# Kernel optimization log

Measured on AMD Instinct MI355X. Metric: run time of the kernel, lower is better.

## Reference

```python
import jax, jax.numpy as jnp
import numpy as np

GRID = (32, 32, 32)  # must match init grid_size


def setup_inputs() -> dict:
    key = jax.random.key(0)
    # Mimic the module's init: D = 0.01 everywhere + 0.1 on the 6x6 diagonal,
    # plus small uniform noise so the baseline exercises non-degenerate values.
    D = jax.random.uniform(key, (6, 6, *GRID), dtype=jnp.float32) * 0.02 + 0.01
    D = D.at[jnp.arange(6), jnp.arange(6)].add(0.1)
    return {"D": D, "sx": 1, "sy": 1, "sz": 1, "ex": 30, "ey": 30, "ez": 30,
            "max_iterations": 300}


def reference(D, sx, sy, sz, ex, ey, ez, max_iterations):
    """flash_wave (training path, inference=False): 300-step CA as one lax.scan.

    Returns the stacked history of phi (pre-update, as the torch loop appends
    phi at the top of each iteration): shape [max_iterations, 6, X, Y, Z].
    Early exit is emulated by freezing phi once the wave reaches (ex,ey,ez),
    so no per-step host sync is needed.
    """
    phi0 = jnp.zeros((6, *GRID), dtype=D.dtype).at[:, sx, sy, sz].set(1.0)
    active_D = D + 0.95  # inference=False branch

    def body(carry, _):
        phi, done = carry
        # 6x6 channel mixing per grid cell: 'oixyz,ixyz->oxyz'
        phi_out = jnp.einsum('oixyz,ixyz->oxyz', active_D, phi)
        pn = jnp.zeros_like(phi)
        pn = pn.at[0, 1:, :, :].set(phi_out[0, :-1, :, :])   # +x
        pn = pn.at[1, :-1, :, :].set(phi_out[1, 1:, :, :])   # -x
        pn = pn.at[2, :, 1:, :].set(phi_out[2, :, :-1, :])   # +y
        pn = pn.at[3, :, :-1, :].set(phi_out[3, :, 1:, :])   # -y
        pn = pn.at[4, :, :, 1:].set(phi_out[4, :, :, :-1])   # +z
        pn = pn.at[5, :, :, :-1].set(phi_out[5, :, :, 1:])   # -z
        nxt = jnp.clip(pn, 0.0, 1.0)
        nxt = jnp.where(done, phi, nxt)  # freeze after target reached
        reached = jnp.sum(nxt[:, ex, ey, ez]) > 0.01
        return (nxt, jnp.logical_or(done, reached)), phi

    (_, _), history = jax.lax.scan(body, (phi0, jnp.array(False)), None,
                                   length=int(max_iterations))
    return history
```

## Files before the change

### kernel.cpp

```cpp
#include <hip/hip_runtime.h>

#define NCH 6
#define NX 32
#define PLANE 1024
#define NCELL (NX * PLANE)
#define STEP_STRIDE (NCH * NCELL)
#define NTHREADS 256
#define NBLOCKS 128
#define RB 2

#define RING_WORDS ((size_t)RB * 3 * NCELL)
#define F_DONE 0

typedef unsigned long long u64;

__device__ __forceinline__ u64 ld64(const u64* p) {
    return __hip_atomic_load(p, __ATOMIC_RELAXED, __HIP_MEMORY_SCOPE_SYSTEM);
}
__device__ __forceinline__ void st64(u64* p, u64 v) {
    __hip_atomic_store(p, v, __ATOMIC_RELAXED, __HIP_MEMORY_SCOPE_SYSTEM);
}
__device__ __forceinline__ int ldi(const int* p) {
    return __hip_atomic_load(p, __ATOMIC_RELAXED, __HIP_MEMORY_SCOPE_SYSTEM);
}
__device__ __forceinline__ void sti(int* p, int v) {
    __hip_atomic_store(p, v, __ATOMIC_RELAXED, __HIP_MEMORY_SCOPE_SYSTEM);
}
__device__ __forceinline__ u64 pack2p(float a, float b, unsigned P) {
    const u64 w = ((u64)__float_as_uint(b) << 32) | __float_as_uint(a);
    return P ? (w | 0x8000000080000000ULL) : w;
}
__device__ __forceinline__ bool tagok(u64 w, unsigned P) {
    return (((unsigned)(w >> 63)) == P) & ((((unsigned)w) >> 31) == P);
}
__device__ __forceinline__ void unpack2(u64 w, float* d0, float* d1) {
    *d0 = __uint_as_float((unsigned)w & 0x7fffffffu);
    *d1 = __uint_as_float((unsigned)(w >> 32) & 0x7fffffffu);
}

__global__ void __launch_bounds__(NTHREADS)
BEMNA_V7_2_PhaseSpace_44117904064519_kernel(
    const float* __restrict__ D,
    const int* __restrict__ sx_p, const int* __restrict__ sy_p,
    const int* __restrict__ sz_p, const int* __restrict__ ex_p,
    const int* __restrict__ ey_p, const int* __restrict__ ez_p,
    const int* __restrict__ maxit_p,
    float* __restrict__ out,
    u64* __restrict__ ring,
    int* __restrict__ flags)
{
    __shared__ float tile[2][NCH][NTHREADS];
    __shared__ int lds_dn;
    volatile int* vdn = &lds_dn;

    const int tid = (int)threadIdx.x;
    const int bx  = (int)blockIdx.x;
    const int x   = bx >> 2;
    const int s   = bx & 3;
    const int yl  = tid >> 5;
    const int z   = tid & 31;
    const int y   = (s << 3) + yl;
    const int cell = (x << 10) + (y << 5) + z;

    const int sx = *sx_p, sy = *sy_p, sz = *sz_p;
    const int ex = *ex_p, ey = *ey_p, ez = *ez_p;
    const int maxit = *maxit_p;
    const bool is_seed   = (cell == ((sx << 10) | (sy << 5) | sz));
    const bool is_target = (cell == ((ex << 10) | (ey << 5) | ez));

    const int  nbg[NCH] = { cell - PLANE, cell + PLANE, cell - 32, cell + 32, cell - 1, cell + 1 };
    const bool ok[NCH]  = { x >= 1, x <= 30, y >= 1, y <= 30, z >= 1, z <= 30 };
    const int izm = (tid - 1) & (NTHREADS - 1), izp = (tid + 1) & (NTHREADS - 1);

    const bool has_xm = (x >= 1), has_xp = (x <= 30);
    const bool has_ym = (yl == 0) && (y >= 1);
    const bool has_yp = (yl == 7) && (y <= 30);

    float dreg[NCH][NCH];
#pragma unroll
    for (int o = 0; o < NCH; ++o)
#pragma unroll
        for (int i = 0; i < NCH; ++i)
            dreg[o][i] = ok[o] ? D[(size_t)(o * NCH + i) * NCELL + nbg[o]] + 0.95f : 0.0f;

    const float iv = is_seed ? 1.0f : 0.0f;
    {
        const u64 p = pack2p(iv, iv, 0);
        st64(&ring[0 * NCELL + cell], p);
        st64(&ring[1 * NCELL + cell], p);
        st64(&ring[2 * NCELL + cell], p);
        float* outp = out + cell;
#pragma unroll
        for (int o = 0; o < NCH; ++o) { outp[o * NCELL] = iv; tile[0][o][tid] = iv; }
    }
    if (tid == 0) lds_dn = -1;
    __syncthreads();

    int tripped = 0;
    for (int t = 0; t <= maxit - 2; ++t) {
        const u64* r0 = ring + (size_t)(t & 1) * 3 * NCELL;
        const u64* r1 = r0 + NCELL;
        const u64* r2 = r1 + NCELL;
        const unsigned P = (unsigned)((t >> 1) & 1);
        const int cm = cell - PLANE, cp = cell + PLANE;
        const int am = cell - 32,    ap = cell + 32;

        u64 wa0 = 0, wa1 = 0, wa2 = 0, wb0 = 0, wb1 = 0, wb2 = 0;
        u64 wc0 = 0, wc1 = 0, wc2 = 0, wd0 = 0, wd1 = 0, wd2 = 0;
        for (;;) {
            if (has_xm) { wa0 = ld64(r0 + cm); wa1 = ld64(r1 + cm); wa2 = ld64(r2 + cm); }
            if (has_xp) { wb0 = ld64(r0 + cp); wb1 = ld64(r1 + cp); wb2 = ld64(r2 + cp); }
            if (has_ym) { wc0 = ld64(r0 + am); wc1 = ld64(r1 + am); wc2 = ld64(r2 + am); }
            if (has_yp) { wd0 = ld64(r0 + ap); wd1 = ld64(r1 + ap); wd2 = ld64(r2 + ap); }
            if ((tid & 63) == 0) {
                const int dn = ldi(&flags[F_DONE]);
                if (dn >= 0) *vdn = dn;
            }
            bool okr = true;
            if (has_xm) okr = okr & tagok(wa0, P) & tagok(wa1, P) & tagok(wa2, P);
            if (has_xp) okr = okr & tagok(wb0, P) & tagok(wb1, P) & tagok(wb2, P);
            if (has_ym) okr = okr & tagok(wc0, P) & tagok(wc1, P) & tagok(wc2, P);
            if (has_yp) okr = okr & tagok(wd0, P) & tagok(wd1, P) & tagok(wd2, P);
            const int d = *vdn;
            if (d >= 0 && t + 1 > d) break;
            if (__ballot(okr) == ~0ull) break;
            __builtin_amdgcn_s_sleep(1);
        }
        __syncthreads();
        { const int d = *vdn; if (d >= 0 && t + 1 > d) break; }

        float xm[NCH], xp[NCH], ym[NCH], yp[NCH];
        unpack2(wa0, &xm[0], &xm[1]); unpack2(wa1, &xm[2], &xm[3]); unpack2(wa2, &xm[4], &xm[5]);
        unpack2(wb0, &xp[0], &xp[1]); unpack2(wb1, &xp[2], &xp[3]); unpack2(wb2, &xp[4], &xp[5]);
        unpack2(wc0, &ym[0], &ym[1]); unpack2(wc1, &ym[2], &ym[3]); unpack2(wc2, &ym[4], &ym[5]);
        unpack2(wd0, &yp[0], &yp[1]); unpack2(wd1, &yp[2], &yp[3]); unpack2(wd2, &yp[4], &yp[5]);

        const float (*L)[NTHREADS] = tile[t & 1];
        if (!has_ym) {
            const int n = (tid - 32) & (NTHREADS - 1);
#pragma unroll
            for (int i = 0; i < NCH; ++i) ym[i] = L[i][n];
        }
        if (!has_yp) {
            const int n = (tid + 32) & (NTHREADS - 1);
#pragma unroll
            for (int i = 0; i < NCH; ++i) yp[i] = L[i][n];
        }

        float v[NCH];
        {
            float a0 = 0.f, a1 = 0.f, a2 = 0.f, a3 = 0.f, a4 = 0.f, a5 = 0.f;
#pragma unroll
            for (int i = 0; i < NCH; ++i) {
                a0 = fmaf(dreg[0][i], xm[i], a0);
                a1 = fmaf(dreg[1][i], xp[i], a1);
                a2 = fmaf(dreg[2][i], ym[i], a2);
                a3 = fmaf(dreg[3][i], yp[i], a3);
                a4 = fmaf(dreg[4][i], L[i][izm], a4);
                a5 = fmaf(dreg[5][i], L[i][izp], a5);
            }
            v[0] = fminf(fmaxf(a0, 0.f), 1.f);
            v[1] = fminf(fmaxf(a1, 0.f), 1.f);
            v[2] = fminf(fmaxf(a2, 0.f), 1.f);
            v[3] = fminf(fmaxf(a3, 0.f), 1.f);
            v[4] = fminf(fmaxf(a4, 0.f), 1.f);
            v[5] = fminf(fmaxf(a5, 0.f), 1.f);
        }

        if (is_target && !tripped) {
            if (v[0] + v[1] + v[2] + v[3] + v[4] + v[5] > 0.01f) {
                sti(&flags[F_DONE], t + 1);
                tripped = 1;
            }
        }

        {
            const unsigned P1 = (unsigned)(((t + 1) >> 1) & 1);
            u64* w0 = ring + (size_t)((t + 1) & 1) * 3 * NCELL;
            st64(w0 + 0 * NCELL + cell, pack2p(v[0], v[1], P1));
            st64(w0 + 1 * NCELL + cell, pack2p(v[2], v[3], P1));
            st64(w0 + 2 * NCELL + cell, pack2p(v[4], v[5], P1));
#pragma unroll
            for (int o = 0; o < NCH; ++o) tile[(t + 1) & 1][o][tid] = v[o];
        }

        {
            float* outp = out + (size_t)(t + 1) * STEP_STRIDE + cell;
#pragma unroll
            for (int o = 0; o < NCH; ++o) outp[o * NCELL] = v[o];
        }
    }
}

__global__ void fill_kernel(const int* __restrict__ flags,
                            float4* __restrict__ out,
                            int total4)
{
    const int s4 = STEP_STRIDE / 4;
    const int maxit = total4 / s4;
    const int ds = flags[F_DONE];
    const int tf = (ds >= 1 && ds <= maxit - 1) ? ds : maxit - 1;
    const int idx = (int)blockIdx.x * (int)blockDim.x + (int)threadIdx.x;
    const float4 v = out[(size_t)tf * s4 + idx];
    for (int t = tf + 1; t < maxit; ++t)
        out[(size_t)t * s4 + idx] = v;
}

extern "C" void kernel_launch(void* const* d_in, const int* in_sizes, int n_in,
                              void* d_out, int out_size, void* d_ws, size_t ws_size,
                              hipStream_t stream)
{
    const float* D   = (const float*)d_in[0];
    const int* sx    = (const int*)d_in[1];
    const int* sy    = (const int*)d_in[2];
    const int* sz    = (const int*)d_in[3];
    const int* ex    = (const int*)d_in[4];
    const int* ey    = (const int*)d_in[5];
    const int* ez    = (const int*)d_in[6];
    const int* maxit = (const int*)d_in[7];
    float* out = (float*)d_out;

    u64* ring  = (u64*)d_ws;
    int* flags = (int*)(ring + RING_WORDS);

    BEMNA_V7_2_PhaseSpace_44117904064519_kernel<<<dim3(NBLOCKS), dim3(NTHREADS), 0, stream>>>(
        D, sx, sy, sz, ex, ey, ez, maxit, out, ring, flags);

    const int total4 = out_size / 4;
    fill_kernel<<<dim3((STEP_STRIDE / 4) / 256), dim3(256), 0, stream>>>(
        flags, (float4*)out, total4);
}
```

Before: 403.1 us.

## Map one x-plane per 1024-thread block to keep y-halo in LDS

Changes the decomposition from 128 blocks of 256 threads (quarter planes) to 32 blocks of 1024 threads, one full x-plane each. The y-neighbour exchange now comes from shared memory instead of tag-polled global ring loads, which cuts global traffic and inter-block spin dependencies. In exchange only 32 CUs are used, and __syncthreads spans 16 waves, so per-step barrier latency and any straggling wave cost more.

```diff
diff --git a/kernel.cpp b/kernel.cpp
--- a/kernel.cpp
+++ b/kernel.cpp
@@ -5,8 +5,8 @@
 #define PLANE 1024
 #define NCELL (NX * PLANE)
 #define STEP_STRIDE (NCH * NCELL)
-#define NTHREADS 256
-#define NBLOCKS 128
+#define NTHREADS 1024
+#define NBLOCKS 32
 #define RB 2
 
 #define RING_WORDS ((size_t)RB * 3 * NCELL)
@@ -54,13 +54,10 @@
     volatile int* vdn = &lds_dn;
 
     const int tid = (int)threadIdx.x;
-    const int bx  = (int)blockIdx.x;
-    const int x   = bx >> 2;
-    const int s   = bx & 3;
-    const int yl  = tid >> 5;
+    const int x   = (int)blockIdx.x;
+    const int y   = tid >> 5;
     const int z   = tid & 31;
-    const int y   = (s << 3) + yl;
-    const int cell = (x << 10) + (y << 5) + z;
+    const int cell = (x << 10) + tid;
 
     const int sx = *sx_p, sy = *sy_p, sz = *sz_p;
     const int ex = *ex_p, ey = *ey_p, ez = *ez_p;
@@ -70,11 +67,10 @@
 
     const int  nbg[NCH] = { cell - PLANE, cell + PLANE, cell - 32, cell + 32, cell - 1, cell + 1 };
     const bool ok[NCH]  = { x >= 1, x <= 30, y >= 1, y <= 30, z >= 1, z <= 30 };
-    const int izm = (tid - 1) & (NTHREADS - 1), izp = (tid + 1) & (NTHREADS - 1);
+    const int izm = (tid - 1)  & (NTHREADS - 1), izp = (tid + 1)  & (NTHREADS - 1);
+    const int iym = (tid - 32) & (NTHREADS - 1), iyp = (tid + 32) & (NTHREADS - 1);
 
     const bool has_xm = (x >= 1), has_xp = (x <= 30);
-    const bool has_ym = (yl == 0) && (y >= 1);
-    const bool has_yp = (yl == 7) && (y <= 30);
 
     float dreg[NCH][NCH];
 #pragma unroll
@@ -103,15 +99,11 @@
         const u64* r2 = r1 + NCELL;
         const unsigned P = (unsigned)((t >> 1) & 1);
         const int cm = cell - PLANE, cp = cell + PLANE;
-        const int am = cell - 32,    ap = cell + 32;
 
         u64 wa0 = 0, wa1 = 0, wa2 = 0, wb0 = 0, wb1 = 0, wb2 = 0;
-        u64 wc0 = 0, wc1 = 0, wc2 = 0, wd0 = 0, wd1 = 0, wd2 = 0;
         for (;;) {
             if (has_xm) { wa0 = ld64(r0 + cm); wa1 = ld64(r1 + cm); wa2 = ld64(r2 + cm); }
             if (has_xp) { wb0 = ld64(r0 + cp); wb1 = ld64(r1 + cp); wb2 = ld64(r2 + cp); }
-            if (has_ym) { wc0 = ld64(r0 + am); wc1 = ld64(r1 + am); wc2 = ld64(r2 + am); }
-            if (has_yp) { wd0 = ld64(r0 + ap); wd1 = ld64(r1 + ap); wd2 = ld64(r2 + ap); }
             if ((tid & 63) == 0) {
                 const int dn = ldi(&flags[F_DONE]);
                 if (dn >= 0) *vdn = dn;
@@ -119,8 +111,6 @@
             bool okr = true;
             if (has_xm) okr = okr & tagok(wa0, P) & tagok(wa1, P) & tagok(wa2, P);
             if (has_xp) okr = okr & tagok(wb0, P) & tagok(wb1, P) & tagok(wb2, P);
-            if (has_ym) okr = okr & tagok(wc0, P) & tagok(wc1, P) & tagok(wc2, P);
-            if (has_yp) okr = okr & tagok(wd0, P) & tagok(wd1, P) & tagok(wd2, P);
             const int d = *vdn;
             if (d >= 0 && t + 1 > d) break;
             if (__ballot(okr) == ~0ull) break;
@@ -129,23 +119,11 @@
         __syncthreads();
         { const int d = *vdn; if (d >= 0 && t + 1 > d) break; }
 
-        float xm[NCH], xp[NCH], ym[NCH], yp[NCH];
+        float xm[NCH], xp[NCH];
         unpack2(wa0, &xm[0], &xm[1]); unpack2(wa1, &xm[2], &xm[3]); unpack2(wa2, &xm[4], &xm[5]);
         unpack2(wb0, &xp[0], &xp[1]); unpack2(wb1, &xp[2], &xp[3]); unpack2(wb2, &xp[4], &xp[5]);
-        unpack2(wc0, &ym[0], &ym[1]); unpack2(wc1, &ym[2], &ym[3]); unpack2(wc2, &ym[4], &ym[5]);
-        unpack2(wd0, &yp[0], &yp[1]); unpack2(wd1, &yp[2], &yp[3]); unpack2(wd2, &yp[4], &yp[5]);
 
         const float (*L)[NTHREADS] = tile[t & 1];
-        if (!has_ym) {
-            const int n = (tid - 32) & (NTHREADS - 1);
-#pragma unroll
-            for (int i = 0; i < NCH; ++i) ym[i] = L[i][n];
-        }
-        if (!has_yp) {
-            const int n = (tid + 32) & (NTHREADS - 1);
-#pragma unroll
-            for (int i = 0; i < NCH; ++i) yp[i] = L[i][n];
-        }
 
         float v[NCH];
         {
@@ -154,8 +132,8 @@
             for (int i = 0; i < NCH; ++i) {
                 a0 = fmaf(dreg[0][i], xm[i], a0);
                 a1 = fmaf(dreg[1][i], xp[i], a1);
-                a2 = fmaf(dreg[2][i], ym[i], a2);
-                a3 = fmaf(dreg[3][i], yp[i], a3);
+                a2 = fmaf(dreg[2][i], L[i][iym], a2);
+                a3 = fmaf(dreg[3][i], L[i][iyp], a3);
                 a4 = fmaf(dreg[4][i], L[i][izm], a4);
                 a5 = fmaf(dreg[5][i], L[i][izp], a5);
             }
```

Result: slower. 469.5 us (+16.5%).

## Shrink blocks to one wavefront and spread grid over more blocks

Applied to the files above, without the earlier changes.

The persistent stencil kernel now runs 512 blocks of 64 threads, each covering two y-rows of one x-plane, instead of 128 blocks of 256 threads. With a single wavefront per block, the done-flag is read by every lane and the LDS broadcast slot is dropped, and the in-block y-neighbour becomes the other row (tid^32). The aim is more parallel workers per step and a cheaper intra-block barrier. In exchange, many more blocks poll the global ring, since more y-neighbours are now fetched from global memory rather than LDS, and all 512 blocks must be co-resident for the spin-wait to make progress.

```diff
diff --git a/kernel.cpp b/kernel.cpp
--- a/kernel.cpp
+++ b/kernel.cpp
@@ -5,8 +5,8 @@
 #define PLANE 1024
 #define NCELL (NX * PLANE)
 #define STEP_STRIDE (NCH * NCELL)
-#define NTHREADS 256
-#define NBLOCKS 128
+#define NTHREADS 64
+#define NBLOCKS 512
 #define RB 2
 
 #define RING_WORDS ((size_t)RB * 3 * NCELL)
@@ -50,16 +50,14 @@
     int* __restrict__ flags)
 {
     __shared__ float tile[2][NCH][NTHREADS];
-    __shared__ int lds_dn;
-    volatile int* vdn = &lds_dn;
 
     const int tid = (int)threadIdx.x;
     const int bx  = (int)blockIdx.x;
-    const int x   = bx >> 2;
-    const int s   = bx & 3;
+    const int x   = bx >> 4;
+    const int p   = bx & 15;
     const int yl  = tid >> 5;
     const int z   = tid & 31;
-    const int y   = (s << 3) + yl;
+    const int y   = (p << 1) | yl;
     const int cell = (x << 10) + (y << 5) + z;
 
     const int sx = *sx_p, sy = *sy_p, sz = *sz_p;
@@ -71,10 +69,11 @@
     const int  nbg[NCH] = { cell - PLANE, cell + PLANE, cell - 32, cell + 32, cell - 1, cell + 1 };
     const bool ok[NCH]  = { x >= 1, x <= 30, y >= 1, y <= 30, z >= 1, z <= 30 };
     const int izm = (tid - 1) & (NTHREADS - 1), izp = (tid + 1) & (NTHREADS - 1);
+    const int iyo = tid ^ 32;
 
     const bool has_xm = (x >= 1), has_xp = (x <= 30);
     const bool has_ym = (yl == 0) && (y >= 1);
-    const bool has_yp = (yl == 7) && (y <= 30);
+    const bool has_yp = (yl == 1) && (y <= 30);
 
     float dreg[NCH][NCH];
 #pragma unroll
@@ -85,15 +84,14 @@
 
     const float iv = is_seed ? 1.0f : 0.0f;
     {
-        const u64 p = pack2p(iv, iv, 0);
-        st64(&ring[0 * NCELL + cell], p);
-        st64(&ring[1 * NCELL + cell], p);
-        st64(&ring[2 * NCELL + cell], p);
+        const u64 pk = pack2p(iv, iv, 0);
+        st64(&ring[0 * NCELL + cell], pk);
+        st64(&ring[1 * NCELL + cell], pk);
+        st64(&ring[2 * NCELL + cell], pk);
         float* outp = out + cell;
 #pragma unroll
         for (int o = 0; o < NCH; ++o) { outp[o * NCELL] = iv; tile[0][o][tid] = iv; }
     }
-    if (tid == 0) lds_dn = -1;
     __syncthreads();
 
     int tripped = 0;
@@ -107,27 +105,24 @@
 
         u64 wa0 = 0, wa1 = 0, wa2 = 0, wb0 = 0, wb1 = 0, wb2 = 0;
         u64 wc0 = 0, wc1 = 0, wc2 = 0, wd0 = 0, wd1 = 0, wd2 = 0;
+        int dabort = 0;
         for (;;) {
             if (has_xm) { wa0 = ld64(r0 + cm); wa1 = ld64(r1 + cm); wa2 = ld64(r2 + cm); }
             if (has_xp) { wb0 = ld64(r0 + cp); wb1 = ld64(r1 + cp); wb2 = ld64(r2 + cp); }
             if (has_ym) { wc0 = ld64(r0 + am); wc1 = ld64(r1 + am); wc2 = ld64(r2 + am); }
             if (has_yp) { wd0 = ld64(r0 + ap); wd1 = ld64(r1 + ap); wd2 = ld64(r2 + ap); }
-            if ((tid & 63) == 0) {
-                const int dn = ldi(&flags[F_DONE]);
-                if (dn >= 0) *vdn = dn;
-            }
+            const int dn = ldi(&flags[F_DONE]);
             bool okr = true;
             if (has_xm) okr = okr & tagok(wa0, P) & tagok(wa1, P) & tagok(wa2, P);
             if (has_xp) okr = okr & tagok(wb0, P) & tagok(wb1, P) & tagok(wb2, P);
             if (has_ym) okr = okr & tagok(wc0, P) & tagok(wc1, P) & tagok(wc2, P);
             if (has_yp) okr = okr & tagok(wd0, P) & tagok(wd1, P) & tagok(wd2, P);
-            const int d = *vdn;
-            if (d >= 0 && t + 1 > d) break;
+            if (dn >= 0 && t + 1 > dn) { dabort = 1; break; }
             if (__ballot(okr) == ~0ull) break;
             __builtin_amdgcn_s_sleep(1);
         }
         __syncthreads();
-        { const int d = *vdn; if (d >= 0 && t + 1 > d) break; }
+        if (dabort) break;
 
         float xm[NCH], xp[NCH], ym[NCH], yp[NCH];
         unpack2(wa0, &xm[0], &xm[1]); unpack2(wa1, &xm[2], &xm[3]); unpack2(wa2, &xm[4], &xm[5]);
@@ -137,14 +132,12 @@
 
         const float (*L)[NTHREADS] = tile[t & 1];
         if (!has_ym) {
-            const int n = (tid - 32) & (NTHREADS - 1);
-#pragma unroll
-            for (int i = 0; i < NCH; ++i) ym[i] = L[i][n];
+#pragma unroll
+            for (int i = 0; i < NCH; ++i) ym[i] = L[i][iyo];
         }
         if (!has_yp) {
-            const int n = (tid + 32) & (NTHREADS - 1);
-#pragma unroll
-            for (int i = 0; i < NCH; ++i) yp[i] = L[i][n];
+#pragma unroll
+            for (int i = 0; i < NCH; ++i) yp[i] = L[i][iyo];
         }
 
         float v[NCH];
```

After: 410.1 us. Within noise of the previous version (+1.7%).
